# Optimization experiments

Hardware: AMD Instinct MI355X
Metric: run time of the kernel (lower is better)

Reference implementation:

```python
import jax, jax.numpy as jnp
import numpy as np

NSIDE = 128
LMAX = 4 * NSIDE - 1            # nlat = 511 (lmax default)
MMAX = (4 * NSIDE) // 2 + 1     # nlon//2 + 1 = 257
NPIX = 12 * NSIDE * NSIDE       # 196608 HEALPix pixels
PAD = 8 * NSIDE                 # Bluestein padding (power of two >= 2*max nphi)


def _ring_geometry(nside):
    """Static HEALPix ring layout: pixels per ring, ring offsets, phi of pixel 0."""
    ntheta = 4 * nside - 1
    t = np.arange(ntheta)
    nphi = np.where(t < nside - 1, 4 * (t + 1),
           np.where(t <= 3 * nside - 1, 4 * nside, 4 * (4 * nside - 1 - t))).astype(np.int64)
    cum = np.concatenate([[0], np.cumsum(nphi)[:-1]]).astype(np.int64)
    phi0 = np.empty(ntheta)
    for tt in range(ntheta):
        if nside - 1 <= tt <= 3 * nside - 1:      # equatorial belt
            shift = 0.5 * ((tt - nside + 2) % 2)
            factor = np.pi / (2 * nside)
        elif tt + 1 > 3 * nside:                  # south polar cap
            shift = 0.5
            factor = np.pi / (2 * (4 * nside - tt - 1))
        else:                                     # north polar cap
            shift = 0.5
            factor = np.pi / (2 * (tt + 1))
        phi0[tt] = factor * shift
    return nphi, cum, phi0


def setup_inputs() -> dict:
    key = jax.random.key(0)
    k1, k2, k3 = jax.random.split(key, 3)
    x_re = jax.random.normal(k1, (LMAX, MMAX), jnp.float32)
    x_im = jax.random.normal(k2, (LMAX, MMAX), jnp.float32)
    # pct stands in for the precomputed associated-Legendre table (mmax, lmax, nlat)
    pct = jax.random.normal(k3, (MMAX, LMAX, LMAX), jnp.float32) * 0.02
    return {"x_re": x_re, "x_im": x_im, "pct": pct}


def reference(x_re, x_im, pct):
    nside = NSIDE
    L = pct.shape[0]                     # mmax
    nphi, cum, phi0 = _ring_geometry(nside)
    n = np.arange(PAD)

    # inverse Legendre transform: ftm[k, m] = sum_l x[l, m] * pct[m, l, k]
    rl = jnp.einsum('lm,mlk->km', x_re, pct)
    im = jnp.einsum('lm,mlk->km', x_im, pct)
    ftm = (rl + 1j * im).astype(jnp.complex64)            # (ntheta, L)

    # per-ring phase shift exp(i*m*phi_ring_offset)  (static chirp)
    phase = np.exp(1j * np.arange(L)[None, :] * phi0[:, None]).astype(np.complex64)
    ftm = ftm * phase

    # conjugated hermitian extension of each ring spectrum to length nphi (zero padded to PAD)
    half = nphi // 2 + 1
    head = n[None, :] < half[:, None]
    in_ring = n[None, :] < nphi[:, None]
    idx = np.where(head, n[None, :], nphi[:, None] - n[None, :])
    valid = in_ring & (idx >= 0) & (idx < L)
    idx_c = np.clip(idx, 0, L - 1)
    g = jnp.take_along_axis(ftm, jnp.asarray(idx_c), axis=1)  # (ntheta, PAD)
    fm_full = jnp.where(valid, jnp.where(jnp.asarray(head), jnp.conj(g), g), 0.0)

    # Bluestein chirps (static, per-ring modulus nphi)
    coef = np.pi * n[None, :] ** 2 / nphi[:, None]
    chirp_a = np.where(in_ring, np.exp(1j * coef), 0).astype(np.complex64)
    chirp_b = np.where(in_ring, np.exp(-1j * coef), 0).astype(np.complex64)
    tail = n[None, :] >= PAD - nphi[:, None] + 1
    tail_coef = np.pi * (PAD - n[None, :]) ** 2 / nphi[:, None]
    y_pad = chirp_a + np.where(tail, np.exp(1j * tail_coef), 0).astype(np.complex64)

    # chirp-z via circular convolution: batched over all rings at once
    x_pad = fm_full * jnp.asarray(chirp_b)
    conv = jnp.fft.ifft(jnp.fft.fft(x_pad, axis=-1) * jnp.fft.fft(jnp.asarray(y_pad), axis=-1), axis=-1)
    vals = jnp.real(conv * jnp.asarray(chirp_b))          # (ntheta, PAD)

    # scatter ring values into the flat HEALPix map (out-of-ring slots -> dump index NPIX)
    pix = np.where(in_ring, cum[:, None] + n[None, :], NPIX).reshape(-1)
    f = jnp.zeros(NPIX + 1, jnp.float32).at[jnp.asarray(pix)].set(vals.reshape(-1).astype(jnp.float32))
    return f[:NPIX]
```

## Files before the change

kernel.cpp:

```cpp
#include <hip/hip_runtime.h>
#include <math.h>

#ifndef M_PI
#define M_PI 3.14159265358979323846
#endif

#define NSIDE  128
#define NTHETA 511
#define MMAX   257
#define NPIX   196608

__global__ __launch_bounds__(256)
void ftm_kernel(const float* __restrict__ x_re,
                const float* __restrict__ x_im,
                const float* __restrict__ pct,
                float* __restrict__ ftm_re,
                float* __restrict__ ftm_im)
{
    __shared__ float xr[NTHETA];
    __shared__ float xi[NTHETA];
    const int m   = blockIdx.y;
    const int tid = threadIdx.x;
    for (int i = tid; i < NTHETA; i += 256) {
        xr[i] = x_re[(size_t)i * MMAX + m];
        xi[i] = x_im[(size_t)i * MMAX + m];
    }
    __syncthreads();
    const int k = blockIdx.x * 256 + tid;
    if (k >= NTHETA) return;

    const float* p = pct + (size_t)m * NTHETA * NTHETA + k;
    float ar = 0.f, ai = 0.f;

    for (int l = 0; l < 496; l += 16) {
        float v[16];
        #pragma unroll
        for (int u = 0; u < 16; ++u) v[u] = p[(size_t)(l + u) * NTHETA];
        #pragma unroll
        for (int u = 0; u < 16; ++u) {
            ar = fmaf(xr[l + u], v[u], ar);
            ai = fmaf(xi[l + u], v[u], ai);
        }
    }
    {
        float v[15];
        #pragma unroll
        for (int u = 0; u < 15; ++u) v[u] = p[(size_t)(496 + u) * NTHETA];
        #pragma unroll
        for (int u = 0; u < 15; ++u) {
            ar = fmaf(xr[496 + u], v[u], ar);
            ai = fmaf(xi[496 + u], v[u], ai);
        }
    }

    ftm_re[(size_t)k * MMAX + m] = ar;
    ftm_im[(size_t)k * MMAX + m] = ai;
}

__global__ __launch_bounds__(256)
void ring_kernel(const float* __restrict__ ftm_re,
                 const float* __restrict__ ftm_im,
                 float* __restrict__ out)
{
    const int t = blockIdx.y;
    int nphi, cum;
    double phi0;
    if (t < NSIDE - 1) {
        nphi = 4 * (t + 1);
        cum  = 2 * t * (t + 1);
        phi0 = M_PI / (4.0 * (t + 1));
    } else if (t <= 3 * NSIDE - 1) {
        nphi = 4 * NSIDE;
        cum  = 2 * (NSIDE - 1) * NSIDE + (t - (NSIDE - 1)) * 4 * NSIDE;
        phi0 = (M_PI / (2.0 * NSIDE)) * (0.5 * (double)((t - NSIDE + 2) % 2));
    } else {
        int s = 4 * NSIDE - 1 - t;
        nphi = 4 * s;
        cum  = NPIX - 2 * s * (s + 1);
        phi0 = M_PI / (4.0 * s);
    }
    if ((int)blockIdx.x * 256 >= nphi) return;

    const int mtop = nphi / 2;
    __shared__ float fr[MMAX];
    __shared__ float fi[MMAX];
    for (int i = threadIdx.x; i <= mtop; i += 256) {
        fr[i] = ftm_re[(size_t)t * MMAX + i];
        fi[i] = ftm_im[(size_t)t * MMAX + i];
    }
    __syncthreads();

    const int k = blockIdx.x * 256 + threadIdx.x;
    if (k >= nphi) return;

    double phi = phi0 + (2.0 * M_PI) * ((double)k / (double)nphi);
    float sp, cp;
    sincosf((float)phi, &sp, &cp);

    float cr = 1.f, ci = 0.f;
    float acc = fr[0];
    for (int m = 1; m < mtop; ++m) {
        float nr = cr * cp - ci * sp;
        float ni = cr * sp + ci * cp;
        cr = nr; ci = ni;
        acc += 2.f * (fr[m] * cr - fi[m] * ci);
    }
    {
        float nr = cr * cp - ci * sp;
        float ni = cr * sp + ci * cp;
        acc += fr[mtop] * nr - fi[mtop] * ni;
    }
    out[cum + k] = acc;
}

extern "C" void kernel_launch(void* const* d_in, const int* in_sizes, int n_in,
                              void* d_out, int out_size, void* d_ws, size_t ws_size,
                              hipStream_t stream)
{
    const float* x_re = (const float*)d_in[0];
    const float* x_im = (const float*)d_in[1];
    const float* pct  = (const float*)d_in[2];
    float* out = (float*)d_out;

    float* ftm_re = (float*)d_ws;
    float* ftm_im = ftm_re + (size_t)NTHETA * MMAX;

    ftm_kernel<<<dim3(2, MMAX), 256, 0, stream>>>(x_re, x_im, pct, ftm_re, ftm_im);
    ring_kernel<<<dim3(2, NTHETA), 256, 0, stream>>>(ftm_re, ftm_im, out);
}
```

Baseline: 71.69 us.

## Split Legendre reduction over l-chunks with aligned float4 pct loads

Replaces the per-(m, k-block) Legendre kernel with a split-K version. Each block handles one m and a 64-row slice of l, and each wave streams aligned float4 rows of pct with per-row shift handling, accumulating into shared-memory bins. Partial sums go to a workspace and are reduced by a separate combine kernel, with a small cleanup kernel for the few edge elements the alignment scheme misses. The goal is more parallelism and wider, aligned loads over the 135 MB pct stream, at the cost of two extra launches and extra partial-sum traffic. The ftm layout also becomes m-major, so the ring kernel now does strided reads.

After: 80.05 us. +11.7%, slower.

```diff
diff --git a/kernel.cpp b/kernel.cpp
--- a/kernel.cpp
+++ b/kernel.cpp
@@ -9,58 +9,167 @@
 #define NTHETA 511
 #define MMAX   257
 #define NPIX   196608
+#define PCT_M  ((size_t)NTHETA * NTHETA)
+#define MN     ((size_t)MMAX * NTHETA)
+#define BINW   544
+#define QSPLIT 8
+
+typedef float4 f4;
+
+template<int S>
+__device__ __forceinline__ void do_row(const float* __restrict__ Pf,
+                                       float2 xv, bool lane0, bool lane63,
+                                       float (&ar)[2][7], float (&ai)[2][7])
+{
+    f4 a0 = *(const f4*)Pf;
+    f4 a1 = *(const f4*)(Pf + 256);
+    if constexpr (S >= 1) { if (lane0)  a0.x = 0.f; }
+    if constexpr (S >= 2) { if (lane0)  a0.y = 0.f; }
+    if constexpr (S >= 3) { if (lane0)  a0.z = 0.f; }
+    if constexpr (S == 0) { if (lane63) a1.w = 0.f; }
+    ar[0][3-S] = fmaf(a0.x, xv.x, ar[0][3-S]);  ai[0][3-S] = fmaf(a0.x, xv.y, ai[0][3-S]);
+    ar[0][4-S] = fmaf(a0.y, xv.x, ar[0][4-S]);  ai[0][4-S] = fmaf(a0.y, xv.y, ai[0][4-S]);
+    ar[0][5-S] = fmaf(a0.z, xv.x, ar[0][5-S]);  ai[0][5-S] = fmaf(a0.z, xv.y, ai[0][5-S]);
+    ar[0][6-S] = fmaf(a0.w, xv.x, ar[0][6-S]);  ai[0][6-S] = fmaf(a0.w, xv.y, ai[0][6-S]);
+    ar[1][3-S] = fmaf(a1.x, xv.x, ar[1][3-S]);  ai[1][3-S] = fmaf(a1.x, xv.y, ai[1][3-S]);
+    ar[1][4-S] = fmaf(a1.y, xv.x, ar[1][4-S]);  ai[1][4-S] = fmaf(a1.y, xv.y, ai[1][4-S]);
+    ar[1][5-S] = fmaf(a1.z, xv.x, ar[1][5-S]);  ai[1][5-S] = fmaf(a1.z, xv.y, ai[1][5-S]);
+    ar[1][6-S] = fmaf(a1.w, xv.x, ar[1][6-S]);  ai[1][6-S] = fmaf(a1.w, xv.y, ai[1][6-S]);
+}
+
+template<int S0>
+__device__ __forceinline__ void wave_loop(const float* __restrict__ pm,
+                                          int lstart, int nrows, int lane,
+                                          const float2* __restrict__ xs, int xbase,
+                                          float (&ar)[2][7], float (&ai)[2][7])
+{
+    constexpr int S1 = (S0 + 3) & 3, S2 = (S0 + 2) & 3, S3 = (S0 + 1) & 3;
+    constexpr int I0 = (S0 == 0) ? 508 : 512;
+    constexpr int I1 = (S1 == 0) ? 508 : 512;
+    constexpr int I2 = (S2 == 0) ? 508 : 512;
+    constexpr int I3 = (S3 == 0) ? 508 : 512;
+    const bool lane0 = (lane == 0), lane63 = (lane == 63);
+    const float* Pf = pm + (size_t)lstart * NTHETA - S0 + lane * 4;
+    int l = lstart - xbase;
+    const int ng = nrows >> 2;
+    for (int g = 0; g < ng; ++g) {
+        do_row<S0>(Pf, xs[l  ], lane0, lane63, ar, ai);  Pf += I0;
+        do_row<S1>(Pf, xs[l+1], lane0, lane63, ar, ai);  Pf += I1;
+        do_row<S2>(Pf, xs[l+2], lane0, lane63, ar, ai);  Pf += I2;
+        do_row<S3>(Pf, xs[l+3], lane0, lane63, ar, ai);  Pf += I3;
+        l += 4;
+    }
+    if (nrows & 3) {
+        do_row<S0>(Pf, xs[l  ], lane0, lane63, ar, ai);  Pf += I0;
+        do_row<S1>(Pf, xs[l+1], lane0, lane63, ar, ai);  Pf += I1;
+        do_row<S2>(Pf, xs[l+2], lane0, lane63, ar, ai);
+    }
+}
+
+__global__ __launch_bounds__(128)
+void ftm_main(const float* __restrict__ x_re, const float* __restrict__ x_im,
+              const float* __restrict__ pct, float* __restrict__ ftm_p)
+{
+    __shared__ float2 xs[64];
+    __shared__ float  bins[2][2][BINW];
+    const int m = blockIdx.x >> 3;
+    const int q = blockIdx.x & 7;
+    const int tid = threadIdx.x;
+    const int w = tid >> 6, lane = tid & 63;
+    const int rbase = q * 64;
+    const int rcount = min(64, NTHETA - rbase);
+
+    if (tid < rcount) {
+        int l = rbase + tid;
+        xs[tid] = make_float2(x_re[(size_t)l * MMAX + m], x_im[(size_t)l * MMAX + m]);
+    }
+    for (int i = tid; i < 2 * 2 * BINW; i += 128) ((float*)bins)[i] = 0.f;
+    __syncthreads();
+
+    const int lstart = rbase + w * 32;
+    const int nrows  = min(32, NTHETA - lstart);
+
+    float ar[2][7], ai[2][7];
+    #pragma unroll
+    for (int h = 0; h < 2; ++h)
+        #pragma unroll
+        for (int c = 0; c < 7; ++c) { ar[h][c] = 0.f; ai[h][c] = 0.f; }
+
+    const float* pm = pct + (size_t)m * PCT_M;
+    switch (m & 3) {
+        case 0: wave_loop<0>(pm, lstart, nrows, lane, xs, rbase, ar, ai); break;
+        case 1: wave_loop<1>(pm, lstart, nrows, lane, xs, rbase, ar, ai); break;
+        case 2: wave_loop<2>(pm, lstart, nrows, lane, xs, rbase, ar, ai); break;
+        case 3: wave_loop<3>(pm, lstart, nrows, lane, xs, rbase, ar, ai); break;
+    }
+
+    #pragma unroll
+    for (int h = 0; h < 2; ++h)
+        #pragma unroll
+        for (int c = 0; c < 7; ++c) {
+            int W = h * 256 + 4 * lane + c;
+            int idx = W + (W >> 5);
+            bins[w][0][idx] += ar[h][c];
+            bins[w][1][idx] += ai[h][c];
+        }
+    __syncthreads();
+
+    float* dst = ftm_p + ((size_t)(q * 2) * MMAX + m) * NTHETA;
+    for (int t = tid; t < NTHETA; t += 128) {
+        int W = t + 3, idx = W + (W >> 5);
+        dst[t]      = bins[0][0][idx] + bins[1][0][idx];
+        dst[MN + t] = bins[0][1][idx] + bins[1][1][idx];
+    }
+}
+
+__global__ __launch_bounds__(640)
+void cleanup(const float* __restrict__ x_re, const float* __restrict__ x_im,
+             const float* __restrict__ pct, float* __restrict__ extra)
+{
+    const int job = threadIdx.x >> 6;
+    const int lane = threadIdx.x & 63;
+    const int tt = job / 5;
+    const int m  = job % 5;
+    const int t  = 509 + tt;
+    float sre = 0.f, sim = 0.f;
+    for (int l = lane; l < NTHETA; l += 64) {
+        int s = (m + 3 * l) & 3;
+        bool take = tt ? (s >= 2) : (s == 3);
+        if (take) {
+            float v = pct[(size_t)m * PCT_M + (size_t)l * NTHETA + t];
+            sre += x_re[(size_t)l * MMAX + m] * v;
+            sim += x_im[(size_t)l * MMAX + m] * v;
+        }
+    }
+    #pragma unroll
+    for (int off = 32; off; off >>= 1) {
+        sre += __shfl_down(sre, off);
+        sim += __shfl_down(sim, off);
+    }
+    if (lane == 0) {
+        extra[(0 * 2 + tt) * 5 + m] = sre;
+        extra[(1 * 2 + tt) * 5 + m] = sim;
+    }
+}
 
 __global__ __launch_bounds__(256)
-void ftm_kernel(const float* __restrict__ x_re,
-                const float* __restrict__ x_im,
-                const float* __restrict__ pct,
-                float* __restrict__ ftm_re,
-                float* __restrict__ ftm_im)
-{
-    __shared__ float xr[NTHETA];
-    __shared__ float xi[NTHETA];
-    const int m   = blockIdx.y;
-    const int tid = threadIdx.x;
-    for (int i = tid; i < NTHETA; i += 256) {
-        xr[i] = x_re[(size_t)i * MMAX + m];
-        xi[i] = x_im[(size_t)i * MMAX + m];
-    }
-    __syncthreads();
-    const int k = blockIdx.x * 256 + tid;
-    if (k >= NTHETA) return;
-
-    const float* p = pct + (size_t)m * NTHETA * NTHETA + k;
-    float ar = 0.f, ai = 0.f;
-
-    for (int l = 0; l < 496; l += 16) {
-        float v[16];
-        #pragma unroll
-        for (int u = 0; u < 16; ++u) v[u] = p[(size_t)(l + u) * NTHETA];
-        #pragma unroll
-        for (int u = 0; u < 16; ++u) {
-            ar = fmaf(xr[l + u], v[u], ar);
-            ai = fmaf(xi[l + u], v[u], ai);
-        }
-    }
-    {
-        float v[15];
-        #pragma unroll
-        for (int u = 0; u < 15; ++u) v[u] = p[(size_t)(496 + u) * NTHETA];
-        #pragma unroll
-        for (int u = 0; u < 15; ++u) {
-            ar = fmaf(xr[496 + u], v[u], ar);
-            ai = fmaf(xi[496 + u], v[u], ai);
-        }
-    }
-
-    ftm_re[(size_t)k * MMAX + m] = ar;
-    ftm_im[(size_t)k * MMAX + m] = ai;
+void combine(const float* __restrict__ ftm_p, const float* __restrict__ extra,
+             float* __restrict__ ftm_c)
+{
+    const size_t i = (size_t)blockIdx.x * 256 + threadIdx.x;
+    if (i >= 2 * MN) return;
+    const int reim = (int)(i / MN);
+    const size_t rem = i % MN;
+    const int m = (int)(rem / NTHETA), t = (int)(rem % NTHETA);
+    float s = 0.f;
+    #pragma unroll
+    for (int q = 0; q < QSPLIT; ++q) s += ftm_p[(size_t)(q * 2 + reim) * MN + rem];
+    if (t >= 509 && m <= 4) s += extra[(reim * 2 + (t - 509)) * 5 + m];
+    ftm_c[i] = s;
 }
 
 __global__ __launch_bounds__(256)
-void ring_kernel(const float* __restrict__ ftm_re,
-                 const float* __restrict__ ftm_im,
-                 float* __restrict__ out)
+void ring_kernel(const float* __restrict__ ftm_c, float* __restrict__ out)
 {
     const int t = blockIdx.y;
     int nphi, cum;
@@ -85,8 +194,8 @@
     __shared__ float fr[MMAX];
     __shared__ float fi[MMAX];
     for (int i = threadIdx.x; i <= mtop; i += 256) {
-        fr[i] = ftm_re[(size_t)t * MMAX + i];
-        fi[i] = ftm_im[(size_t)t * MMAX + i];
+        fr[i] = ftm_c[(size_t)i * NTHETA + t];
+        fi[i] = ftm_c[MN + (size_t)i * NTHETA + t];
     }
     __syncthreads();
 
@@ -99,11 +208,11 @@
 
     float cr = 1.f, ci = 0.f;
     float acc = fr[0];
-    for (int m = 1; m < mtop; ++m) {
+    for (int mm = 1; mm < mtop; ++mm) {
         float nr = cr * cp - ci * sp;
         float ni = cr * sp + ci * cp;
         cr = nr; ci = ni;
-        acc += 2.f * (fr[m] * cr - fi[m] * ci);
+        acc += 2.f * (fr[mm] * cr - fi[mm] * ci);
     }
     {
         float nr = cr * cp - ci * sp;
@@ -122,9 +231,12 @@
     const float* pct  = (const float*)d_in[2];
     float* out = (float*)d_out;
 
-    float* ftm_re = (float*)d_ws;
-    float* ftm_im = ftm_re + (size_t)NTHETA * MMAX;
-
-    ftm_kernel<<<dim3(2, MMAX), 256, 0, stream>>>(x_re, x_im, pct, ftm_re, ftm_im);
-    ring_kernel<<<dim3(2, NTHETA), 256, 0, stream>>>(ftm_re, ftm_im, out);
-}
+    float* ftm_p = (float*)d_ws;
+    float* ftm_c = ftm_p + (size_t)QSPLIT * 2 * MN;
+    float* extra = ftm_c + 2 * MN;
+
+    ftm_main<<<dim3(MMAX * QSPLIT), 128, 0, stream>>>(x_re, x_im, pct, ftm_p);
+    cleanup <<<dim3(1), 640, 0, stream>>>(x_re, x_im, pct, extra);
+    combine <<<dim3((unsigned)((2 * MN + 255) / 256)), 256, 0, stream>>>(ftm_p, extra, ftm_c);
+    ring_kernel<<<dim3(2, NTHETA), 256, 0, stream>>>(ftm_c, out);
+}
```
